# Kernel optimization log

Hardware: AMD Instinct MI355X
Metric: run time of the kernel (lower is better)

The kernel has to match this reference:

```python
import jax, jax.numpy as jnp
import numpy as np

B, CIN, COUT, H, W = 8, 64, 64, 96, 96
K = 3
PAD = 1
BN_EPS = 1e-5


def conv2d(x, w, b):
    # plain 3x3 conv, stride 1, pad 1 (NCHW / OIHW)
    y = jax.lax.conv_general_dilated(
        x, w, window_strides=(1, 1), padding=[(PAD, PAD), (PAD, PAD)],
        dimension_numbers=("NCHW", "OIHW", "NCHW"))
    return y + b[None, :, None, None]


def setup_inputs() -> dict:
    key = jax.random.key(0)
    ks = jax.random.split(key, 6)
    s = 0.05  # small init so offsets stay near the regular grid (matches DCN zero-ish init)
    return {
        "x": jax.random.normal(ks[0], (B, CIN, H, W), jnp.float32),
        "offset_w": jax.random.normal(ks[1], (2 * K * K, CIN, K, K), jnp.float32) * s,
        "offset_b": jnp.zeros((2 * K * K,), jnp.float32),
        "mod_w": jax.random.normal(ks[2], (K * K, CIN, K, K), jnp.float32) * s,
        "mod_b": jnp.zeros((K * K,), jnp.float32),
        "weight": jax.random.normal(ks[3], (COUT, CIN, K, K), jnp.float32) * s,
        "bias": jax.random.normal(ks[4], (COUT,), jnp.float32) * s,
        "bn_gamma": jnp.ones((COUT,), jnp.float32),
        "bn_beta": jnp.zeros((COUT,), jnp.float32),
        "bn_mean": jnp.zeros((COUT,), jnp.float32),
        "bn_var": jnp.ones((COUT,), jnp.float32),
    }


def _deform_sample(xb, py, px):
    # xb: [C,H,W]; py, px: [K2,H,W] fractional sampling coords (zero outside image)
    y0 = jnp.floor(py)
    x0 = jnp.floor(px)
    dy = py - y0
    dx = px - x0

    def gather(yi, xi):
        valid = ((yi >= 0) & (yi < H) & (xi >= 0) & (xi < W)).astype(xb.dtype)
        yc = jnp.clip(yi, 0, H - 1).astype(jnp.int32)
        xc = jnp.clip(xi, 0, W - 1).astype(jnp.int32)
        return xb[:, yc, xc] * valid  # [C,K2,H,W]

    v00 = gather(y0, x0)
    v01 = gather(y0, x0 + 1.0)
    v10 = gather(y0 + 1.0, x0)
    v11 = gather(y0 + 1.0, x0 + 1.0)
    return (v00 * (1 - dy) * (1 - dx) + v01 * (1 - dy) * dx
            + v10 * dy * (1 - dx) + v11 * dy * dx)  # [C,K2,H,W]


def reference(x, offset_w, offset_b, mod_w, mod_b, weight, bias,
              bn_gamma, bn_beta, bn_mean, bn_var):
    # 1) predict offsets and modulation mask (DCNv2)
    offset = conv2d(x, offset_w, offset_b)                 # [B, 2*K2, H, W]
    modulator = 2.0 * jax.nn.sigmoid(conv2d(x, mod_w, mod_b))  # [B, K2, H, W]

    off = offset.reshape(B, K * K, 2, H, W)
    off_y, off_x = off[:, :, 0], off[:, :, 1]              # [B,K2,H,W]

    # 2) base sampling grid per kernel tap
    ky, kx = jnp.meshgrid(jnp.arange(K), jnp.arange(K), indexing="ij")
    base_y = (jnp.arange(H)[None, :, None] - PAD
              + ky.reshape(-1)[:, None, None]).astype(jnp.float32)  # [K2,H,1]
    base_x = (jnp.arange(W)[None, None, :] - PAD
              + kx.reshape(-1)[:, None, None]).astype(jnp.float32)  # [K2,1,W]
    py = base_y + off_y                                    # [B,K2,H,W]
    px = base_x + off_x

    # 3) bilinear gather at irregular positions, modulate per tap
    sampled = jax.vmap(_deform_sample)(x, py, px)          # [B,C,K2,H,W]
    sampled = sampled * modulator[:, None]                 # broadcast over C

    # 4) contract taps with the regular conv weight
    wk = weight.reshape(COUT, CIN, K * K)
    y = jnp.einsum("bckhw,ock->bohw", sampled, wk) + bias[None, :, None, None]

    # 5) BatchNorm (inference: running stats) + ReLU
    inv = bn_gamma / jnp.sqrt(bn_var + BN_EPS)
    y = (y - bn_mean[None, :, None, None]) * inv[None, :, None, None] \
        + bn_beta[None, :, None, None]
    return jax.nn.relu(y)
```

## Files before the change

### kernel.cpp

```cpp
#include <hip/hip_runtime.h>
#include <hip/hip_bf16.h>
#include <hip/hip_fp16.h>
#include <math.h>

#define BB 8
#define HH 96
#define WW 96
#define HW 9216
#define BN_EPS 1e-5f

typedef _Float16 f16x2 __attribute__((ext_vector_type(2)));
typedef _Float16 f16x8 __attribute__((ext_vector_type(8)));
typedef float f32x4 __attribute__((ext_vector_type(4)));

union HU  { _Float16 h; unsigned short u; };
union UH2 { unsigned u; f16x2 h; };
union U4H { uint4 u; f16x2 h2[4]; };

#define OFF_XT   0
#define SZ_XT    (BB*HW*64*2)
#define OFF_WB   (OFF_XT + SZ_XT)
#define SZ_WB    (64*576*2)
#define OFF_WO   (OFF_WB + SZ_WB)
#define SZ_WO    (32*576*2)
#define OFF_BN   (OFF_WO + SZ_WO)
#define SZ_BN    (64*2*4)

__global__ __launch_bounds__(256) void prep_kernel(
    const float* __restrict__ weight, const float* __restrict__ offw,
    const float* __restrict__ modw,
    const float* __restrict__ bias, const float* __restrict__ gamma,
    const float* __restrict__ beta, const float* __restrict__ mean,
    const float* __restrict__ var,
    _Float16* __restrict__ wB, _Float16* __restrict__ wOff,
    float* __restrict__ bnS, float* __restrict__ bnB) {
  int tid = blockIdx.x * 256 + threadIdx.x;
  if (tid < 64 * 576) {
    int o = tid / 576, ck = tid % 576;
    int k = ck >> 6, c = ck & 63;
    wB[tid] = (_Float16)weight[o * 576 + c * 9 + k];
  }
  int t2 = tid - 64 * 576;
  if (t2 >= 0 && t2 < 32 * 576) {
    int oc = t2 / 576, kcol = t2 % 576;
    int kk = kcol >> 6, c = kcol & 63;
    float v = 0.f;
    if (oc < 18)      v = offw[(oc * 64 + c) * 9 + kk];
    else if (oc < 27) v = modw[((oc - 18) * 64 + c) * 9 + kk];
    wOff[t2] = (_Float16)v;
  }
  int t3 = tid - (64 * 576 + 32 * 576);
  if (t3 >= 0 && t3 < 64) {
    float inv = gamma[t3] * rsqrtf(var[t3] + BN_EPS);
    bnS[t3] = inv;
    bnB[t3] = (bias[t3] - mean[t3]) * inv + beta[t3];
  }
}

__global__ __launch_bounds__(256) void transpose_x_kernel(
    const float* __restrict__ x, _Float16* __restrict__ xT) {
  __shared__ float tile[64][65];
  int tid = threadIdx.x;
  int b = blockIdx.x & 7;
  int hwb = (blockIdx.x >> 3) * 64;
  int col = tid & 63, g = tid >> 6;
  float r[16];
#pragma unroll
  for (int it = 0; it < 16; ++it)
    r[it] = x[(b * 64 + it * 4 + g) * HW + hwb + col];
  __builtin_amdgcn_sched_barrier(0);
#pragma unroll
  for (int it = 0; it < 16; ++it)
    tile[it * 4 + g][col] = r[it];
  __syncthreads();
#pragma unroll
  for (int it = 0; it < 16; ++it) {
    int p = it * 4 + g;
    xT[(size_t)(b * HW + hwb + p) * 64 + col] = (_Float16)tile[col][p];
  }
}

__device__ __forceinline__ unsigned rep16(float w) {
  HU cv; cv.h = (_Float16)w;
  return 0x10001u * (unsigned)cv.u;
}

__global__ __launch_bounds__(256, 6) void dcn_fused_kernel(
    const _Float16* __restrict__ xT, const _Float16* __restrict__ wOff,
    const float* __restrict__ offb, const float* __restrict__ modb,
    const _Float16* __restrict__ wB,
    const float* __restrict__ bnS, const float* __restrict__ bnB,
    float* __restrict__ out) {
  __shared__ __attribute__((aligned(16))) char uLDS[18688];
  __shared__ unsigned xys[144];
  __shared__ __attribute__((aligned(16))) uint4 w4s[144];
  _Float16* sN     = (_Float16*)uLDS;
  float*    o_part = (float*)(uLDS + 7776);
  _Float16* s_A    = (_Float16*)uLDS;
  float*    o_lds  = (float*)uLDS;

  int tid = threadIdx.x;
  int lane = tid & 63;
  int wv = __builtin_amdgcn_readfirstlane(tid >> 6);

  int bi = blockIdx.x;
  int b = bi & 7, t = bi >> 3;
  int h = t / 6, w0 = (t - (t / 6) * 6) * 16;
  int hwrow = h * WW + w0;

  const _Float16* xb = xT + (size_t)b * HW * 64;
  const unsigned char* xbc = (const unsigned char*)xb;

  _Float16 sv[14];
#pragma unroll
  for (int i = 0; i < 14; ++i) {
    int p = wv + 4 * i;
    _Float16 v = (_Float16)0.f;
    if (p < 54) {
      int row = p / 18, col = p - row * 18;
      int y = h + row - 1, xx = w0 + col - 1;
      if ((y >= 0) && (y < HH) && (xx >= 0) && (xx < WW))
        v = xb[(size_t)(y * WW + xx) * 64 + lane];
    }
    sv[i] = v;
  }
  __builtin_amdgcn_sched_barrier(0);
#pragma unroll
  for (int i = 0; i < 14; ++i) {
    int p = wv + 4 * i;
    if (p < 54) sN[p * 72 + lane] = sv[i];
  }
  __syncthreads();

  int r = lane & 15, g = lane >> 4;
  {
    int nt = wv & 1, ks = wv >> 1;
    const _Float16* bp = wOff + (nt * 16 + r) * 576 + ks * 288 + g * 8;
    f32x4 acc = {0.f, 0.f, 0.f, 0.f};
#pragma unroll
    for (int si = 0; si < 9; ++si) {
      int s = ks * 9 + si;
      int kk = s >> 1, ky = kk / 3, kx = kk - ky * 3, ch = s & 1;
      f16x8 a  = *(const f16x8*)&sN[(ky * 18 + r + kx) * 72 + ch * 32 + g * 8];
      f16x8 bb = *(const f16x8*)(bp + si * 32);
      acc = __builtin_amdgcn_mfma_f32_16x16x32_f16(a, bb, acc, 0, 0, 0);
    }
#pragma unroll
    for (int j = 0; j < 4; ++j)
      o_part[ks * 528 + (g * 4 + j) * 33 + nt * 16 + r] = acc[j];
  }
  __syncthreads();

  if (tid < 144) {
    int px = tid / 9, k = tid - px * 9;
    int ky = k / 3, kx = k - ky * 3;
    int w = w0 + px;
    float offy = o_part[px * 33 + 2 * k]     + o_part[528 + px * 33 + 2 * k]     + offb[2 * k];
    float offx = o_part[px * 33 + 2 * k + 1] + o_part[528 + px * 33 + 2 * k + 1] + offb[2 * k + 1];
    float mz   = o_part[px * 33 + 18 + k]    + o_part[528 + px * 33 + 18 + k]    + modb[k];
    float mod  = 2.f / (1.f + __expf(-mz));

    float py  = (float)(h - 1 + ky) + offy;
    float px_ = (float)(w - 1 + kx) + offx;
    float y0f = floorf(py), x0f = floorf(px_);
    float dy = py - y0f, dx = px_ - x0f;
    int y0 = (int)y0f, x0 = (int)x0f;
    int y1 = y0 + 1, x1 = x0 + 1;
    bool vy0 = (y0 >= 0) && (y0 < HH), vy1 = (y1 >= 0) && (y1 < HH);
    bool vx0 = (x0 >= 0) && (x0 < WW), vx1 = (x1 >= 0) && (x1 < WW);
    float w00 = (vy0 && vx0) ? (1.f - dy) * (1.f - dx) * mod : 0.f;
    float w01 = (vy0 && vx1) ? (1.f - dy) * dx * mod : 0.f;
    float w10 = (vy1 && vx0) ? dy * (1.f - dx) * mod : 0.f;
    float w11 = (vy1 && vx1) ? dy * dx * mod : 0.f;
    int y0c = min(max(y0, 0), HH - 1), y1c = min(max(y1, 0), HH - 1);
    int x0c = min(max(x0, 0), WW - 1), x1c = min(max(x1, 0), WW - 1);
    xys[tid] = (unsigned)y0c | ((unsigned)y1c << 8) |
               ((unsigned)x0c << 16) | ((unsigned)x1c << 24);
    w4s[tid] = make_uint4(rep16(w00), rep16(w01), rep16(w10), rep16(w11));
  }
  __syncthreads();

  int hsel = lane >> 5;
  unsigned ch4 = (unsigned)((lane & 31) << 2);

#pragma unroll
  for (int px = 0; px < 4; ++px) {
    int pl = wv * 4 + px;
    int mi = pl * 9;
    unsigned q[9];
#pragma unroll
    for (int k = 0; k < 9; ++k) q[k] = xys[mi + k];

#pragma unroll
    for (int p4 = 0; p4 < 4; ++p4) {
      const int kA = 2 * p4;
      unsigned qa = q[kA], qb = q[kA + 1];
      unsigned aY0 = qa & 255u, aY1 = (qa >> 8) & 255u;
      unsigned aX0 = (qa >> 16) & 255u, aX1 = qa >> 24;
      unsigned bY0 = qb & 255u, bY1 = (qb >> 8) & 255u;
      unsigned bX0 = (qb >> 16) & 255u, bX1 = qb >> 24;
      unsigned oA0 = (aY0 * WW + aX0) << 7, oA1 = (aY0 * WW + aX1) << 7;
      unsigned oA2 = (aY1 * WW + aX0) << 7, oA3 = (aY1 * WW + aX1) << 7;
      unsigned oB0 = (bY0 * WW + bX0) << 7, oB1 = (bY0 * WW + bX1) << 7;
      unsigned oB2 = (bY1 * WW + bX0) << 7, oB3 = (bY1 * WW + bX1) << 7;
      unsigned a0 = (hsel ? oB0 : oA0) + ch4;
      unsigned a1 = (hsel ? oB1 : oA1) + ch4;
      unsigned a2 = (hsel ? oB2 : oA2) + ch4;
      unsigned a3 = (hsel ? oB3 : oA3) + ch4;
      unsigned t0 = *(const unsigned*)(xbc + a0);
      unsigned t1 = *(const unsigned*)(xbc + a1);
      unsigned t2 = *(const unsigned*)(xbc + a2);
      unsigned t3 = *(const unsigned*)(xbc + a3);
      U4H Wa, Wb;
      Wa.u = w4s[mi + kA]; Wb.u = w4s[mi + kA + 1];
      f16x2 W0 = hsel ? Wb.h2[0] : Wa.h2[0];
      f16x2 W1 = hsel ? Wb.h2[1] : Wa.h2[1];
      f16x2 W2 = hsel ? Wb.h2[2] : Wa.h2[2];
      f16x2 W3 = hsel ? Wb.h2[3] : Wa.h2[3];
      UH2 v0, v1, v2, v3, s;
      v0.u = t0; v1.u = t1; v2.u = t2; v3.u = t3;
      s.h = v0.h * W0 + v1.h * W1 + v2.h * W2 + v3.h * W3;
      *(unsigned*)&s_A[pl * 584 + (kA + hsel) * 64 + (int)(ch4 >> 1)] = s.u;
    }
    {
      unsigned qa = q[8];
      unsigned aY0 = qa & 255u, aY1 = (qa >> 8) & 255u;
      unsigned aX0 = (qa >> 16) & 255u, aX1 = qa >> 24;
      unsigned a0 = (((aY0 * WW + aX0) << 7)) + ch4;
      unsigned a1 = (((aY0 * WW + aX1) << 7)) + ch4;
      unsigned a2 = (((aY1 * WW + aX0) << 7)) + ch4;
      unsigned a3 = (((aY1 * WW + aX1) << 7)) + ch4;
      unsigned t0 = *(const unsigned*)(xbc + a0);
      unsigned t1 = *(const unsigned*)(xbc + a1);
      unsigned t2 = *(const unsigned*)(xbc + a2);
      unsigned t3 = *(const unsigned*)(xbc + a3);
      U4H W; W.u = w4s[mi + 8];
      UH2 v0, v1, v2, v3, s;
      v0.u = t0; v1.u = t1; v2.u = t2; v3.u = t3;
      s.h = v0.h * W.h2[0] + v1.h * W.h2[1] + v2.h * W.h2[2] + v3.h * W.h2[3];
      if (lane < 32)
        *(unsigned*)&s_A[pl * 584 + 512 + (int)(ch4 >> 1)] = s.u;
    }
  }
  __syncthreads();

  const _Float16* arow = s_A + r * 584 + g * 8;
  const _Float16* bp = wB + (wv * 16 + r) * 576 + g * 8;
  f32x4 accA = {0.f, 0.f, 0.f, 0.f}, accB = {0.f, 0.f, 0.f, 0.f};
#pragma unroll 3
  for (int s = 0; s < 18; s += 2) {
    f16x8 a0 = *(const f16x8*)(arow + s * 32);
    f16x8 b0 = *(const f16x8*)(bp + s * 32);
    f16x8 a1 = *(const f16x8*)(arow + s * 32 + 32);
    f16x8 b1 = *(const f16x8*)(bp + s * 32 + 32);
    accA = __builtin_amdgcn_mfma_f32_16x16x32_f16(a0, b0, accA, 0, 0, 0);
    accB = __builtin_amdgcn_mfma_f32_16x16x32_f16(a1, b1, accB, 0, 0, 0);
  }

  int o = wv * 16 + r;
  float sc = bnS[o], sh = bnB[o];
  __syncthreads();
#pragma unroll
  for (int j = 0; j < 4; ++j) {
    int px = g * 4 + j;
    o_lds[o * 20 + px] = fmaxf((accA[j] + accB[j]) * sc + sh, 0.f);
  }
  __syncthreads();

  int oo = tid >> 2, qd = tid & 3;
  float4 u = *(const float4*)&o_lds[oo * 20 + qd * 4];
  *(float4*)(out + (size_t)(b * 64 + oo) * HW + hwrow + qd * 4) = u;
}

extern "C" void kernel_launch(void* const* d_in, const int* in_sizes, int n_in,
                              void* d_out, int out_size, void* d_ws, size_t ws_size,
                              hipStream_t stream) {
  const float* x      = (const float*)d_in[0];
  const float* offw   = (const float*)d_in[1];
  const float* offb   = (const float*)d_in[2];
  const float* modw   = (const float*)d_in[3];
  const float* modb   = (const float*)d_in[4];
  const float* weight = (const float*)d_in[5];
  const float* bias   = (const float*)d_in[6];
  const float* gamma  = (const float*)d_in[7];
  const float* beta   = (const float*)d_in[8];
  const float* mean   = (const float*)d_in[9];
  const float* var    = (const float*)d_in[10];

  char* ws = (char*)d_ws;
  _Float16*  xTh   = (_Float16*)(ws + OFF_XT);
  _Float16*  wB    = (_Float16*)(ws + OFF_WB);
  _Float16*  wOff  = (_Float16*)(ws + OFF_WO);
  float*     bnS   = (float*)(ws + OFF_BN);
  float*     bnB   = bnS + 64;

  prep_kernel<<<217, 256, 0, stream>>>(weight, offw, modw, bias, gamma, beta,
                                       mean, var, wB, wOff, bnS, bnB);
  transpose_x_kernel<<<1152, 256, 0, stream>>>(x, xTh);
  dcn_fused_kernel<<<4608, 256, 0, stream>>>(xTh, wOff, offb, modb, wB,
                                             bnS, bnB, (float*)d_out);
}
```

Baseline: 89.66 us.

## Process 32-pixel row segments per block, processing sample/GEMM in two halves

Each block now covers 32 output pixels instead of 16, halving the grid. The 3x34 halo tile is loaded once into LDS, and the offset/modulator conv runs as two M-tiles with the full K range, with no split-K partial sums. The sampling and main GEMM stages loop over two 16-pixel halves and reuse the same LDS buffers. This cuts redundant halo loads and per-block setup, but adds syncs and a serialized second half per block, and increases LDS use (larger xys/w4s arrays), which may reduce occupancy.

```diff
diff --git a/kernel.cpp b/kernel.cpp
--- a/kernel.cpp
+++ b/kernel.cpp
@@ -92,32 +92,31 @@
     const float* __restrict__ bnS, const float* __restrict__ bnB,
     float* __restrict__ out) {
   __shared__ __attribute__((aligned(16))) char uLDS[18688];
-  __shared__ unsigned xys[144];
-  __shared__ __attribute__((aligned(16))) uint4 w4s[144];
-  _Float16* sN     = (_Float16*)uLDS;
-  float*    o_part = (float*)(uLDS + 7776);
-  _Float16* s_A    = (_Float16*)uLDS;
-  float*    o_lds  = (float*)uLDS;
+  __shared__ unsigned xys[288];
+  __shared__ __attribute__((aligned(16))) uint4 w4s[288];
+  _Float16* sN    = (_Float16*)uLDS;
+  float*    o_off = (float*)(uLDS + 14280);
+  _Float16* s_A   = (_Float16*)uLDS;
+  float*    o_lds = (float*)uLDS;
 
   int tid = threadIdx.x;
   int lane = tid & 63;
   int wv = __builtin_amdgcn_readfirstlane(tid >> 6);
 
   int bi = blockIdx.x;
-  int b = bi & 7, t = bi >> 3;
-  int h = t / 6, w0 = (t - (t / 6) * 6) * 16;
-  int hwrow = h * WW + w0;
+  int b = bi & 7, rem = bi >> 3;
+  int h = rem / 3, w0 = (rem % 3) * 32;
 
   const _Float16* xb = xT + (size_t)b * HW * 64;
   const unsigned char* xbc = (const unsigned char*)xb;
 
-  _Float16 sv[14];
-#pragma unroll
-  for (int i = 0; i < 14; ++i) {
+  _Float16 sv[26];
+#pragma unroll
+  for (int i = 0; i < 26; ++i) {
     int p = wv + 4 * i;
     _Float16 v = (_Float16)0.f;
-    if (p < 54) {
-      int row = p / 18, col = p - row * 18;
+    if (p < 102) {
+      int row = p / 34, col = p - row * 34;
       int y = h + row - 1, xx = w0 + col - 1;
       if ((y >= 0) && (y < HH) && (xx >= 0) && (xx < WW))
         v = xb[(size_t)(y * WW + xx) * 64 + lane];
@@ -126,39 +125,39 @@
   }
   __builtin_amdgcn_sched_barrier(0);
 #pragma unroll
-  for (int i = 0; i < 14; ++i) {
+  for (int i = 0; i < 26; ++i) {
     int p = wv + 4 * i;
-    if (p < 54) sN[p * 72 + lane] = sv[i];
+    if (p < 102) sN[p * 70 + lane] = sv[i];
   }
   __syncthreads();
 
   int r = lane & 15, g = lane >> 4;
   {
-    int nt = wv & 1, ks = wv >> 1;
-    const _Float16* bp = wOff + (nt * 16 + r) * 576 + ks * 288 + g * 8;
+    int mt = wv >> 1, nt = wv & 1;
+    int px = mt * 16 + r;
+    const _Float16* bp = wOff + (nt * 16 + r) * 576 + g * 8;
     f32x4 acc = {0.f, 0.f, 0.f, 0.f};
 #pragma unroll
-    for (int si = 0; si < 9; ++si) {
-      int s = ks * 9 + si;
-      int kk = s >> 1, ky = kk / 3, kx = kk - ky * 3, ch = s & 1;
-      f16x8 a  = *(const f16x8*)&sN[(ky * 18 + r + kx) * 72 + ch * 32 + g * 8];
-      f16x8 bb = *(const f16x8*)(bp + si * 32);
+    for (int s = 0; s < 18; ++s) {
+      int kk = s >> 1, ky = kk / 3, kx = kk - ky * 3;
+      f16x8 a  = *(const f16x8*)&sN[(ky * 34 + px + kx) * 70 + (s & 1) * 32 + g * 8];
+      f16x8 bb = *(const f16x8*)(bp + s * 32);
       acc = __builtin_amdgcn_mfma_f32_16x16x32_f16(a, bb, acc, 0, 0, 0);
     }
 #pragma unroll
     for (int j = 0; j < 4; ++j)
-      o_part[ks * 528 + (g * 4 + j) * 33 + nt * 16 + r] = acc[j];
+      o_off[(mt * 16 + g * 4 + j) * 33 + nt * 16 + r] = acc[j];
   }
   __syncthreads();
 
-  if (tid < 144) {
-    int px = tid / 9, k = tid - px * 9;
+  for (int it = tid; it < 288; it += 256) {
+    int pxx = it & 31, k = it >> 5;
     int ky = k / 3, kx = k - ky * 3;
-    int w = w0 + px;
-    float offy = o_part[px * 33 + 2 * k]     + o_part[528 + px * 33 + 2 * k]     + offb[2 * k];
-    float offx = o_part[px * 33 + 2 * k + 1] + o_part[528 + px * 33 + 2 * k + 1] + offb[2 * k + 1];
-    float mz   = o_part[px * 33 + 18 + k]    + o_part[528 + px * 33 + 18 + k]    + modb[k];
-    float mod  = 2.f / (1.f + __expf(-mz));
+    int w = w0 + pxx;
+
+    float offy = o_off[pxx * 33 + 2 * k]     + offb[2 * k];
+    float offx = o_off[pxx * 33 + 2 * k + 1] + offb[2 * k + 1];
+    float mod  = 2.f / (1.f + __expf(-(o_off[pxx * 33 + 18 + k] + modb[k])));
 
     float py  = (float)(h - 1 + ky) + offy;
     float px_ = (float)(w - 1 + kx) + offx;
@@ -174,102 +173,109 @@
     float w11 = (vy1 && vx1) ? dy * dx * mod : 0.f;
     int y0c = min(max(y0, 0), HH - 1), y1c = min(max(y1, 0), HH - 1);
     int x0c = min(max(x0, 0), WW - 1), x1c = min(max(x1, 0), WW - 1);
-    xys[tid] = (unsigned)y0c | ((unsigned)y1c << 8) |
+    int rec = pxx * 9 + k;
+    xys[rec] = (unsigned)y0c | ((unsigned)y1c << 8) |
                ((unsigned)x0c << 16) | ((unsigned)x1c << 24);
-    w4s[tid] = make_uint4(rep16(w00), rep16(w01), rep16(w10), rep16(w11));
+    w4s[rec] = make_uint4(rep16(w00), rep16(w01), rep16(w10), rep16(w11));
   }
   __syncthreads();
 
   int hsel = lane >> 5;
   unsigned ch4 = (unsigned)((lane & 31) << 2);
-
-#pragma unroll
-  for (int px = 0; px < 4; ++px) {
-    int pl = wv * 4 + px;
-    int mi = pl * 9;
-    unsigned q[9];
-#pragma unroll
-    for (int k = 0; k < 9; ++k) q[k] = xys[mi + k];
-
-#pragma unroll
-    for (int p4 = 0; p4 < 4; ++p4) {
-      const int kA = 2 * p4;
-      unsigned qa = q[kA], qb = q[kA + 1];
-      unsigned aY0 = qa & 255u, aY1 = (qa >> 8) & 255u;
-      unsigned aX0 = (qa >> 16) & 255u, aX1 = qa >> 24;
-      unsigned bY0 = qb & 255u, bY1 = (qb >> 8) & 255u;
-      unsigned bX0 = (qb >> 16) & 255u, bX1 = qb >> 24;
-      unsigned oA0 = (aY0 * WW + aX0) << 7, oA1 = (aY0 * WW + aX1) << 7;
-      unsigned oA2 = (aY1 * WW + aX0) << 7, oA3 = (aY1 * WW + aX1) << 7;
-      unsigned oB0 = (bY0 * WW + bX0) << 7, oB1 = (bY0 * WW + bX1) << 7;
-      unsigned oB2 = (bY1 * WW + bX0) << 7, oB3 = (bY1 * WW + bX1) << 7;
-      unsigned a0 = (hsel ? oB0 : oA0) + ch4;
-      unsigned a1 = (hsel ? oB1 : oA1) + ch4;
-      unsigned a2 = (hsel ? oB2 : oA2) + ch4;
-      unsigned a3 = (hsel ? oB3 : oA3) + ch4;
-      unsigned t0 = *(const unsigned*)(xbc + a0);
-      unsigned t1 = *(const unsigned*)(xbc + a1);
-      unsigned t2 = *(const unsigned*)(xbc + a2);
-      unsigned t3 = *(const unsigned*)(xbc + a3);
-      U4H Wa, Wb;
-      Wa.u = w4s[mi + kA]; Wb.u = w4s[mi + kA + 1];
-      f16x2 W0 = hsel ? Wb.h2[0] : Wa.h2[0];
-      f16x2 W1 = hsel ? Wb.h2[1] : Wa.h2[1];
-      f16x2 W2 = hsel ? Wb.h2[2] : Wa.h2[2];
-      f16x2 W3 = hsel ? Wb.h2[3] : Wa.h2[3];
-      UH2 v0, v1, v2, v3, s;
-      v0.u = t0; v1.u = t1; v2.u = t2; v3.u = t3;
-      s.h = v0.h * W0 + v1.h * W1 + v2.h * W2 + v3.h * W3;
-      *(unsigned*)&s_A[pl * 584 + (kA + hsel) * 64 + (int)(ch4 >> 1)] = s.u;
-    }
-    {
-      unsigned qa = q[8];
-      unsigned aY0 = qa & 255u, aY1 = (qa >> 8) & 255u;
-      unsigned aX0 = (qa >> 16) & 255u, aX1 = qa >> 24;
-      unsigned a0 = (((aY0 * WW + aX0) << 7)) + ch4;
-      unsigned a1 = (((aY0 * WW + aX1) << 7)) + ch4;
-      unsigned a2 = (((aY1 * WW + aX0) << 7)) + ch4;
-      unsigned a3 = (((aY1 * WW + aX1) << 7)) + ch4;
-      unsigned t0 = *(const unsigned*)(xbc + a0);
-      unsigned t1 = *(const unsigned*)(xbc + a1);
-      unsigned t2 = *(const unsigned*)(xbc + a2);
-      unsigned t3 = *(const unsigned*)(xbc + a3);
-      U4H W; W.u = w4s[mi + 8];
-      UH2 v0, v1, v2, v3, s;
-      v0.u = t0; v1.u = t1; v2.u = t2; v3.u = t3;
-      s.h = v0.h * W.h2[0] + v1.h * W.h2[1] + v2.h * W.h2[2] + v3.h * W.h2[3];
-      if (lane < 32)
-        *(unsigned*)&s_A[pl * 584 + 512 + (int)(ch4 >> 1)] = s.u;
-    }
-  }
-  __syncthreads();
-
-  const _Float16* arow = s_A + r * 584 + g * 8;
-  const _Float16* bp = wB + (wv * 16 + r) * 576 + g * 8;
-  f32x4 accA = {0.f, 0.f, 0.f, 0.f}, accB = {0.f, 0.f, 0.f, 0.f};
-#pragma unroll 3
-  for (int s = 0; s < 18; s += 2) {
-    f16x8 a0 = *(const f16x8*)(arow + s * 32);
-    f16x8 b0 = *(const f16x8*)(bp + s * 32);
-    f16x8 a1 = *(const f16x8*)(arow + s * 32 + 32);
-    f16x8 b1 = *(const f16x8*)(bp + s * 32 + 32);
-    accA = __builtin_amdgcn_mfma_f32_16x16x32_f16(a0, b0, accA, 0, 0, 0);
-    accB = __builtin_amdgcn_mfma_f32_16x16x32_f16(a1, b1, accB, 0, 0, 0);
-  }
-
   int o = wv * 16 + r;
   float sc = bnS[o], sh = bnB[o];
-  __syncthreads();
-#pragma unroll
-  for (int j = 0; j < 4; ++j) {
-    int px = g * 4 + j;
-    o_lds[o * 20 + px] = fmaxf((accA[j] + accB[j]) * sc + sh, 0.f);
-  }
-  __syncthreads();
-
-  int oo = tid >> 2, qd = tid & 3;
-  float4 u = *(const float4*)&o_lds[oo * 20 + qd * 4];
-  *(float4*)(out + (size_t)(b * 64 + oo) * HW + hwrow + qd * 4) = u;
+
+  for (int half = 0; half < 2; ++half) {
+    int base16 = half * 16;
+    int hwrow16 = h * WW + w0 + base16;
+
+#pragma unroll
+    for (int px = 0; px < 4; ++px) {
+      int pl = wv * 4 + px;
+      int mi = (base16 + pl) * 9;
+      unsigned q[9];
+#pragma unroll
+      for (int k = 0; k < 9; ++k) q[k] = xys[mi + k];
+
+#pragma unroll
+      for (int p4 = 0; p4 < 4; ++p4) {
+        const int kA = 2 * p4;
+        unsigned qa = q[kA], qb = q[kA + 1];
+        unsigned aY0 = qa & 255u, aY1 = (qa >> 8) & 255u;
+        unsigned aX0 = (qa >> 16) & 255u, aX1 = qa >> 24;
+        unsigned bY0 = qb & 255u, bY1 = (qb >> 8) & 255u;
+        unsigned bX0 = (qb >> 16) & 255u, bX1 = qb >> 24;
+        unsigned oA0 = (aY0 * WW + aX0) << 7, oA1 = (aY0 * WW + aX1) << 7;
+        unsigned oA2 = (aY1 * WW + aX0) << 7, oA3 = (aY1 * WW + aX1) << 7;
+        unsigned oB0 = (bY0 * WW + bX0) << 7, oB1 = (bY0 * WW + bX1) << 7;
+        unsigned oB2 = (bY1 * WW + bX0) << 7, oB3 = (bY1 * WW + bX1) << 7;
+        unsigned a0 = (hsel ? oB0 : oA0) + ch4;
+        unsigned a1 = (hsel ? oB1 : oA1) + ch4;
+        unsigned a2 = (hsel ? oB2 : oA2) + ch4;
+        unsigned a3 = (hsel ? oB3 : oA3) + ch4;
+        unsigned t0 = *(const unsigned*)(xbc + a0);
+        unsigned t1 = *(const unsigned*)(xbc + a1);
+        unsigned t2 = *(const unsigned*)(xbc + a2);
+        unsigned t3 = *(const unsigned*)(xbc + a3);
+        U4H Wa, Wb;
+        Wa.u = w4s[mi + kA]; Wb.u = w4s[mi + kA + 1];
+        f16x2 W0 = hsel ? Wb.h2[0] : Wa.h2[0];
+        f16x2 W1 = hsel ? Wb.h2[1] : Wa.h2[1];
+        f16x2 W2 = hsel ? Wb.h2[2] : Wa.h2[2];
+        f16x2 W3 = hsel ? Wb.h2[3] : Wa.h2[3];
+        UH2 v0, v1, v2, v3, s;
+        v0.u = t0; v1.u = t1; v2.u = t2; v3.u = t3;
+        s.h = v0.h * W0 + v1.h * W1 + v2.h * W2 + v3.h * W3;
+        *(unsigned*)&s_A[pl * 584 + (kA + hsel) * 64 + (int)(ch4 >> 1)] = s.u;
+      }
+      {
+        unsigned qa = q[8];
+        unsigned aY0 = qa & 255u, aY1 = (qa >> 8) & 255u;
+        unsigned aX0 = (qa >> 16) & 255u, aX1 = qa >> 24;
+        unsigned a0 = (((aY0 * WW + aX0) << 7)) + ch4;
+        unsigned a1 = (((aY0 * WW + aX1) << 7)) + ch4;
+        unsigned a2 = (((aY1 * WW + aX0) << 7)) + ch4;
+        unsigned a3 = (((aY1 * WW + aX1) << 7)) + ch4;
+        unsigned t0 = *(const unsigned*)(xbc + a0);
+        unsigned t1 = *(const unsigned*)(xbc + a1);
+        unsigned t2 = *(const unsigned*)(xbc + a2);
+        unsigned t3 = *(const unsigned*)(xbc + a3);
+        U4H W; W.u = w4s[mi + 8];
+        UH2 v0, v1, v2, v3, s;
+        v0.u = t0; v1.u = t1; v2.u = t2; v3.u = t3;
+        s.h = v0.h * W.h2[0] + v1.h * W.h2[1] + v2.h * W.h2[2] + v3.h * W.h2[3];
+        if (lane < 32)
+          *(unsigned*)&s_A[pl * 584 + 512 + (int)(ch4 >> 1)] = s.u;
+      }
+    }
+    __syncthreads();
+
+    const _Float16* arow = s_A + r * 584 + g * 8;
+    const _Float16* bp = wB + (wv * 16 + r) * 576 + g * 8;
+    f32x4 accA = {0.f, 0.f, 0.f, 0.f}, accB = {0.f, 0.f, 0.f, 0.f};
+#pragma unroll 3
+    for (int s = 0; s < 18; s += 2) {
+      f16x8 a0 = *(const f16x8*)(arow + s * 32);
+      f16x8 b0 = *(const f16x8*)(bp + s * 32);
+      f16x8 a1 = *(const f16x8*)(arow + s * 32 + 32);
+      f16x8 b1 = *(const f16x8*)(bp + s * 32 + 32);
+      accA = __builtin_amdgcn_mfma_f32_16x16x32_f16(a0, b0, accA, 0, 0, 0);
+      accB = __builtin_amdgcn_mfma_f32_16x16x32_f16(a1, b1, accB, 0, 0, 0);
+    }
+
+    __syncthreads();
+#pragma unroll
+    for (int j = 0; j < 4; ++j) {
+      int px = g * 4 + j;
+      o_lds[o * 20 + px] = fmaxf((accA[j] + accB[j]) * sc + sh, 0.f);
+    }
+    __syncthreads();
+
+    int oo = tid >> 2, qd = tid & 3;
+    float4 u = *(const float4*)&o_lds[oo * 20 + qd * 4];
+    *(float4*)(out + (size_t)(b * 64 + oo) * HW + hwrow16 + qd * 4) = u;
+    __syncthreads();
+  }
 }
 
 extern "C" void kernel_launch(void* const* d_in, const int* in_sizes, int n_in,
@@ -297,6 +303,6 @@
   prep_kernel<<<217, 256, 0, stream>>>(weight, offw, modw, bias, gamma, beta,
                                        mean, var, wB, wOff, bnS, bnB);
   transpose_x_kernel<<<1152, 256, 0, stream>>>(x, xTh);
-  dcn_fused_kernel<<<4608, 256, 0, stream>>>(xTh, wOff, offb, modb, wB,
+  dcn_fused_kernel<<<2304, 256, 0, stream>>>(xTh, wOff, offb, modb, wB,
                                              bnS, bnB, (float*)d_out);
 }
```

After: 93.72 us. 1.05x slower.
